# Kernel optimization log

Measured on AMD Instinct MI355X. Metric: run time of the kernel, lower is better.

## Reference

```python
import jax, jax.numpy as jnp
import numpy as np

N, DIN, E, BLK = 16384, 128, 262144, 2048
H1, DH1, H2, DH2 = 4, 128, 4, 128
D, L, HT, OUT = 128, 5, 4, 2


def _gat(h_in, src, dst, W, a_s, a_d, b, concat):
    # PyG GATConv (eval mode, no dropout): message src->dst, softmax per dst
    H, Dh = a_s.shape
    h = (h_in @ W).reshape(N, H, Dh)
    als = jnp.einsum('nhd,hd->nh', h, a_s)
    ald = jnp.einsum('nhd,hd->nh', h, a_d)
    e = jax.nn.leaky_relu(als[src] + ald[dst], 0.2)            # [E2,H]
    m = jax.ops.segment_max(e, dst, num_segments=N)
    ex = jnp.exp(e - m[dst])
    den = jax.ops.segment_sum(ex, dst, num_segments=N)
    alpha = ex / (den[dst] + 1e-16)
    out = jax.ops.segment_sum(alpha[:, :, None] * h[src], dst, num_segments=N)
    return (out.reshape(N, H * Dh) if concat else out.mean(axis=1)) + b


def _pe():
    pos = jnp.arange(L, dtype=jnp.float32)[:, None]
    div = jnp.exp(jnp.arange(0, D, 2, dtype=jnp.float32) * (-jnp.log(10000.0) / D))
    return jnp.zeros((L, D)).at[:, 0::2].set(jnp.sin(pos * div)).at[:, 1::2].set(jnp.cos(pos * div))


def reference(x, edge_index, time_step, W1, a_src1, a_dst1, b1, W2, a_src2, a_dst2, b2,
              wq, bq, wk, bk, wv, bv, wo, bo, ln_g, ln_b, f1, fb1, f2, fb2, wc, bc):
    s, d = edge_index[0], edge_index[1]
    loops = jnp.arange(N, dtype=edge_index.dtype)
    src = jnp.concatenate([s, d, loops])
    dst = jnp.concatenate([d, s, loops])

    # structural encoder (two GAT layers)
    h = jax.nn.elu(_gat(x, src, dst, W1, a_src1, a_dst1, b1, True))
    h2 = _gat(h, src, dst, W2, a_src2, a_dst2, b2, False)       # [N, D]

    # temporal self-attention: banks are empty (one snapshot per node), so
    # seq has only the last slot valid; original detaches seq before temporal.
    seq = jnp.zeros((N, L, D), h2.dtype).at[:, L - 1].set(jax.lax.stop_gradient(h2))
    xs = seq + _pe()[None]                                       # [N,L,D]
    dh = D // HT
    q = xs[:, -1]                                                # only last query is used
    Q = (q @ wq + bq).reshape(N, HT, dh)
    K = (xs @ wk + bk).reshape(N, L, HT, dh)
    V = (xs @ wv + bv).reshape(N, L, HT, dh)
    scores = jnp.einsum('nhd,nlhd->nhl', Q, K) / jnp.sqrt(jnp.float32(dh))
    valid = (jnp.arange(L) == L - 1)                             # key_padding_mask: pad except last
    scores = jnp.where(valid[None, None, :], scores, -1e9)
    attn = jax.nn.softmax(scores, axis=-1)
    ctx = jnp.einsum('nhl,nlhd->nhd', attn, V).reshape(N, D)
    ao = ctx @ wo + bo

    def ln(v):
        mu = v.mean(-1, keepdims=True)
        var = v.var(-1, keepdims=True)
        return (v - mu) / jnp.sqrt(var + 1e-5) * ln_g + ln_b

    y = ln(q + ao)
    y = ln(y + jax.nn.relu(y @ f1 + fb1) @ f2 + fb2)
    return y @ wc + bc                                           # [N, 2]


def setup_inputs():
    key = jax.random.key(0)
    ks = jax.random.split(key, 20)
    src = jax.random.randint(ks[0], (E,), 0, N, dtype=jnp.int32)
    off = jax.random.randint(ks[1], (E,), 0, BLK, dtype=jnp.int32)
    dst = (src // BLK) * BLK + off                               # within-snapshot edges
    r = lambda k, shape, s=0.05: jax.random.normal(k, shape, jnp.float32) * s
    return {
        'x': jax.random.normal(ks[2], (N, DIN), jnp.float32),
        'edge_index': jnp.stack([src, dst]),
        'time_step': (jnp.arange(N) // BLK).astype(jnp.int64),
        'W1': r(ks[3], (DIN, H1 * DH1)), 'a_src1': r(ks[4], (H1, DH1)), 'a_dst1': r(ks[5], (H1, DH1)), 'b1': jnp.zeros((H1 * DH1,)),
        'W2': r(ks[6], (H1 * DH1, H2 * DH2)), 'a_src2': r(ks[7], (H2, DH2)), 'a_dst2': r(ks[8], (H2, DH2)), 'b2': jnp.zeros((DH2,)),
        'wq': r(ks[9], (D, D)), 'bq': jnp.zeros((D,)), 'wk': r(ks[10], (D, D)), 'bk': jnp.zeros((D,)),
        'wv': r(ks[11], (D, D)), 'bv': jnp.zeros((D,)), 'wo': r(ks[12], (D, D)), 'bo': jnp.zeros((D,)),
        'ln_g': jnp.ones((D,)), 'ln_b': jnp.zeros((D,)),
        'f1': r(ks[13], (D, 4 * D)), 'fb1': jnp.zeros((4 * D,)), 'f2': r(ks[14], (4 * D, D)), 'fb2': jnp.zeros((D,)),
        'wc': r(ks[15], (D, OUT)), 'bc': jnp.zeros((OUT,)),
    }
```

## Files before the change

### kernel.cpp

```cpp
#include <hip/hip_runtime.h>
#include <hip/hip_bf16.h>

#define NODES 16384
#define FEAT 512
typedef __hip_bfloat16 bf16;
typedef __hip_bfloat162 bf162;
typedef short short8v __attribute__((ext_vector_type(8)));
typedef float f32x4 __attribute__((ext_vector_type(4)));

static __device__ __forceinline__ float b2f(short s){
  return __uint_as_float(((unsigned)(unsigned short)s) << 16);
}
static __device__ __forceinline__ void split_store(bf16* h, bf16* l, size_t i, float v){
  bf16 hi = __float2bfloat16(v);
  h[i] = hi; l[i] = __float2bfloat16(v - __bfloat162float(hi));
}

__global__ void sentinel_kernel(float* __restrict__ out, int n, float v){
  int i = blockIdx.x*blockDim.x + threadIdx.x;
  if (i < n) out[i] = v;
}

__global__ void zero_kernel(int* __restrict__ p, int n){
  int i = blockIdx.x*blockDim.x + threadIdx.x;
  if (i < n) p[i] = 0;
}
__global__ void count_kernel(const int* __restrict__ ei, int* __restrict__ counts, int E){
  int i = blockIdx.x*blockDim.x + threadIdx.x;
  if (i < 2*E){
    int dst = (i < E) ? ei[E+i] : ei[i-E];
    atomicAdd(&counts[dst], 1);
  }
}
__global__ __launch_bounds__(1024) void scan_kernel(const int* __restrict__ counts,
                                                    int* __restrict__ offs, int* __restrict__ cursor){
  __shared__ int sh[1024];
  const int t = threadIdx.x;
  int loc[16]; int s = 0;
#pragma unroll
  for (int i=0;i<16;i++){ loc[i] = counts[t*16+i]; s += loc[i]; }
  sh[t] = s; __syncthreads();
  for (int d=1; d<1024; d<<=1){
    int v = (t>=d) ? sh[t-d] : 0;
    __syncthreads(); sh[t] += v; __syncthreads();
  }
  int run = (t==0) ? 0 : sh[t-1];
#pragma unroll
  for (int i=0;i<16;i++){ offs[t*16+i] = run; cursor[t*16+i] = run; run += loc[i]; }
  if (t==1023) offs[NODES] = run;
}
__global__ void fill_kernel(const int* __restrict__ ei, int* __restrict__ cursor,
                            unsigned short* __restrict__ csr, int E){
  int i = blockIdx.x*blockDim.x + threadIdx.x;
  if (i < 2*E){
    int src = ei[i];
    int dst = (i < E) ? ei[E+i] : ei[i-E];
    int pos = atomicAdd(&cursor[dst], 1);
    csr[pos] = (unsigned short)src;
  }
}

struct PrepArgs {
  const float *x,*W1,*W2,*wv,*wo,*f1,*f2;
  bf16 *xh,*w1h,*w2h,*wvh,*wvl,*woh,*wol,*f1h,*f1l,*f2h,*f2l;
};
__global__ void prep_kernel(PrepArgs P){
  int i = blockIdx.x*blockDim.x + threadIdx.x;
  if (i < 2097152){ P.xh[i] = __float2bfloat16(P.x[i]); return; }
  i -= 2097152;
  if (i < 65536){ P.w1h[i] = __float2bfloat16(P.W1[(i&127)*512 + (i>>7)]); return; }
  i -= 65536;
  if (i < 262144){ P.w2h[i] = __float2bfloat16(P.W2[(i&511)*512 + (i>>9)]); return; }
  i -= 262144;
  if (i < 16384){ split_store(P.wvh, P.wvl, i, P.wv[(i&127)*128 + (i>>7)]); return; }
  i -= 16384;
  if (i < 16384){ split_store(P.woh, P.wol, i, P.wo[(i&127)*128 + (i>>7)]); return; }
  i -= 16384;
  if (i < 65536){ split_store(P.f1h, P.f1l, i, P.f1[(i&127)*512 + (i>>7)]); return; }
  i -= 65536;
  if (i < 65536){ split_store(P.f2h, P.f2l, i, P.f2[(i&511)*128 + (i>>9)]); return; }
}

static __device__ __forceinline__ short8v ld8(const bf16* p){
  return *(const short8v*)(const void*)(p);
}

template<int K>
__global__ __launch_bounds__(256) void lgemm(
    const bf16* __restrict__ A, const bf16* __restrict__ B,
    bf16* __restrict__ C, int N){
  __shared__ bf16 As[128*40];
  __shared__ bf16 Bs[128*40];
  const int tid = threadIdx.x;
  const int l = tid & 63, w = tid >> 6;
  const int lg = l >> 4, lr = l & 15;
  const int wr = w >> 1, wc = w & 1;
  const int r0 = blockIdx.x*128;
  const int c0 = blockIdx.y*128;
  const int srow = tid >> 1;
  const int spos = (tid & 1) * 16;
  f32x4 acc[4][4] = {};
  const int ardA[4] = { (wr*64 +  0 + lr)*40 + lg*8, (wr*64 + 16 + lr)*40 + lg*8,
                        (wr*64 + 32 + lr)*40 + lg*8, (wr*64 + 48 + lr)*40 + lg*8 };
  const int brdB[4] = { (wc*64 +  0 + lr)*40 + lg*8, (wc*64 + 16 + lr)*40 + lg*8,
                        (wc*64 + 32 + lr)*40 + lg*8, (wc*64 + 48 + lr)*40 + lg*8 };
  const size_t agbase = (size_t)(r0 + srow)*K + spos;
  const size_t bgbase = (size_t)(c0 + srow)*K + spos;
  const int sl = srow*40 + spos;
#pragma unroll
  for (int k0 = 0; k0 < K; k0 += 32){
    *(short8v*)&As[sl]     = ld8(A + agbase + k0);
    *(short8v*)&As[sl + 8] = ld8(A + agbase + k0 + 8);
    *(short8v*)&Bs[sl]     = ld8(B + bgbase + k0);
    *(short8v*)&Bs[sl + 8] = ld8(B + bgbase + k0 + 8);
    __syncthreads();
    short8v af[4], bfr[4];
#pragma unroll
    for (int f=0; f<4; f++){
      af[f]  = *(const short8v*)&As[ardA[f]];
      bfr[f] = *(const short8v*)&Bs[brdB[f]];
    }
#pragma unroll
    for (int fm=0; fm<4; fm++)
#pragma unroll
      for (int fn=0; fn<4; fn++)
        acc[fm][fn] = __builtin_amdgcn_mfma_f32_16x16x32_bf16(af[fm], bfr[fn], acc[fm][fn], 0,0,0);
    __syncthreads();
  }
#pragma unroll
  for (int fm=0; fm<4; fm++){
#pragma unroll
    for (int fn=0; fn<4; fn++){
      const int col = c0 + wc*64 + fn*16 + lr;
#pragma unroll
      for (int r=0; r<4; r++){
        const int row = r0 + wr*64 + fm*16 + lg*4 + r;
        C[(size_t)row*N + col] = __float2bfloat16(acc[fm][fn][r]);
      }
    }
  }
}

template<int K, int SA, int SB, int ACT, int OMODE, int WPB>
__global__ __launch_bounds__(256) void mgemm(
    const bf16* __restrict__ Ah, const bf16* __restrict__ Al,
    const bf16* __restrict__ Bh, const bf16* __restrict__ Bl,
    const float* __restrict__ bias,
    float* __restrict__ Cf, bf16* __restrict__ Ch, bf16* __restrict__ Cl, int N){
  const int l = threadIdx.x & 63, w = threadIdx.x >> 6;
  const int lg = l >> 4, lr = l & 15;
  const int r0 = (blockIdx.x*WPB + w)*64;
  const int c0 = blockIdx.y*64;
  f32x4 acc[4][4] = {};
  int abase[4], bbase[4];
#pragma unroll
  for (int f=0; f<4; f++){
    abase[f] = (r0 + f*16 + lr)*K + lg*8;
    bbase[f] = (c0 + f*16 + lr)*K + lg*8;
  }
#pragma unroll
  for (int k0 = 0; k0 < K; k0 += 32){
    short8v ah[4], alo[4], bh[4], blo[4];
#pragma unroll
    for (int f=0; f<4; f++){
      ah[f] = ld8(Ah + abase[f] + k0);
      if (SA) alo[f] = ld8(Al + abase[f] + k0);
      bh[f] = ld8(Bh + bbase[f] + k0);
      if (SB) blo[f] = ld8(Bl + bbase[f] + k0);
    }
#pragma unroll
    for (int fm=0; fm<4; fm++)
#pragma unroll
      for (int fn=0; fn<4; fn++){
        acc[fm][fn] = __builtin_amdgcn_mfma_f32_16x16x32_bf16(ah[fm], bh[fn], acc[fm][fn], 0,0,0);
        if (SB) acc[fm][fn] = __builtin_amdgcn_mfma_f32_16x16x32_bf16(ah[fm], blo[fn], acc[fm][fn], 0,0,0);
        if (SA) acc[fm][fn] = __builtin_amdgcn_mfma_f32_16x16x32_bf16(alo[fm], bh[fn], acc[fm][fn], 0,0,0);
      }
  }
#pragma unroll
  for (int fm=0; fm<4; fm++){
#pragma unroll
    for (int fn=0; fn<4; fn++){
      const int col = c0 + fn*16 + lr;
      const float bv = bias ? bias[col] : 0.f;
#pragma unroll
      for (int r=0; r<4; r++){
        const int row = r0 + fm*16 + lg*4 + r;
        float v = acc[fm][fn][r] + bv;
        if (ACT==1) v = fmaxf(v, 0.f);
        const size_t idx = (size_t)row*N + col;
        if (OMODE==0) Cf[idx] = v;
        else if (OMODE==1) Ch[idx] = __float2bfloat16(v);
        else split_store(Ch, Cl, idx, v);
      }
    }
  }
}

__global__ __launch_bounds__(256) void alsald_kernel(const bf16* __restrict__ h,
    const float* __restrict__ a_s, const float* __restrict__ a_d,
    float* __restrict__ als, float* __restrict__ ald){
  int n = blockIdx.x;
  int w = threadIdx.x >> 6, lane = threadIdx.x & 63;
  int c = w*128 + lane*2;
  bf162 hv = *(const bf162*)&h[(size_t)n*FEAT + c];
  float hx = __bfloat162float(hv.x), hy = __bfloat162float(hv.y);
  float2 as2 = *(const float2*)&a_s[c];
  float2 ad2 = *(const float2*)&a_d[c];
  float s = hx*as2.x + hy*as2.y;
  float d = hx*ad2.x + hy*ad2.y;
#pragma unroll
  for (int o=32;o>0;o>>=1){ s += __shfl_xor(s,o); d += __shfl_xor(d,o); }
  if (lane == 0){ als[n*4+w] = s; ald[n*4+w] = d; }
}

template<bool CONCAT>
__global__ __launch_bounds__(256) void gat_fused_kernel(const bf16* __restrict__ hfeat,
    const float* __restrict__ als, const float* __restrict__ ald,
    const int* __restrict__ offs, const unsigned short* __restrict__ csr,
    const float* __restrict__ bias, void* __restrict__ outv,
    bf16* __restrict__ qh, bf16* __restrict__ ql){
  const int w = threadIdx.x >> 6, l = threadIdx.x & 63, g = l >> 4, s16 = l & 15;
  const int nb = blockIdx.x;
  const int n = (nb & 7)*2048 + (nb >> 3)*4 + w;
  const float adg = ald[(size_t)n*4 + g];
  const int beg = offs[n];
  const int cnt = offs[n+1] - beg + 1;
  float ev[6]; int sv[6];
#pragma unroll
  for (int p=0;p<6;p++){
    const int i = s16 + p*16;
    int src = n;
    float e = -1e30f;
    if (i < cnt){
      if (i < cnt-1) src = (int)csr[beg+i];
      float t = als[(size_t)src*4+g] + adg;
      e = fmaxf(t, 0.2f*t);
    }
    ev[p] = e; sv[p] = src;
  }
  float m = -1e30f;
#pragma unroll
  for (int p=0;p<6;p++) m = fmaxf(m, ev[p]);
  float den = 0.f;
#pragma unroll
  for (int p=0;p<6;p++) den += (ev[p] > -1e29f) ? __expf(ev[p]-m) : 0.f;
#pragma unroll
  for (int mask=1; mask<16; mask<<=1){
    float mo = __shfl_xor(m, mask);
    float dd = __shfl_xor(den, mask);
    float nm = fmaxf(m, mo);
    den = den*__expf(m-nm) + dd*__expf(mo-nm);
    m = nm;
  }
  const float C = __expf(-m)/(den + 1e-16f);
  int pk[6];
#pragma unroll
  for (int p=0;p<6;p++){
    float a = (ev[p] > -1e29f) ? __expf(ev[p])*C : 0.f;
    bf16 ab = __float2bfloat16(a);
    pk[p] = ((int)*(unsigned short*)&ab << 16) | (sv[p] & 0xFFFF);
  }
  float acc[8] = {0,0,0,0,0,0,0,0};
  const int fb = l*8;
  const bf16* hp = hfeat + fb;
#pragma unroll
  for (int p=0;p<6;p++){
    const int pbase = p*16;
    if (pbase < cnt){
      const int lim = (cnt - pbase < 16) ? (cnt - pbase) : 16;
      int u_c = __shfl(pk[p], (l & 48));
      short8v hv_c = *(const short8v*)(const void*)(hp + (size_t)(u_c & 0xFFFF)*FEAT);
      for (int j=1; j<lim; ++j){
        const int u_n = __shfl(pk[p], (l & 48) | j);
        const short8v hv_n = *(const short8v*)(const void*)(hp + (size_t)(u_n & 0xFFFF)*FEAT);
        const float a_c = __uint_as_float((unsigned)u_c & 0xFFFF0000u);
#pragma unroll
        for (int k=0;k<8;k++) acc[k] += a_c * b2f(hv_c[k]);
        u_c = u_n; hv_c = hv_n;
      }
      const float a_c = __uint_as_float((unsigned)u_c & 0xFFFF0000u);
#pragma unroll
      for (int k=0;k<8;k++) acc[k] += a_c * b2f(hv_c[k]);
    }
  }
  for (int i = 96; i < cnt; ++i){
    const int src = (i < cnt-1) ? (int)csr[beg+i] : n;
    float t = als[(size_t)src*4+g] + adg;
    t = fmaxf(t, 0.2f*t);
    const float a = __expf(t)*C;
    const short8v hv = *(const short8v*)(const void*)&hfeat[(size_t)src*FEAT + fb];
#pragma unroll
    for (int k=0;k<8;k++) acc[k] += a * b2f(hv[k]);
  }
  if (CONCAT){
    short8v ov;
#pragma unroll
    for (int j=0;j<8;j++){
      float v = acc[j] + bias[fb+j];
      v = v > 0.f ? v : expm1f(v);
      bf16 bv = __float2bfloat16(v);
      ov[j] = (short)*(unsigned short*)&bv;
    }
    *(short8v*)((char*)outv + ((size_t)n*FEAT + fb)*2) = ov;
  } else {
#pragma unroll
    for (int j=0;j<8;j++){
      acc[j] += __shfl_xor(acc[j], 16);
      acc[j] += __shfl_xor(acc[j], 32);
    }
    if (l < 16){
      float* op = (float*)outv + (size_t)n*128 + l*8;
#pragma unroll
      for (int j=0;j<8;j++){
        const int col = l*8 + j;
        float v = 0.25f*acc[j] + bias[col];
        float ex = __expf((float)(col & ~1) * (-9.210340371976184f/128.f));
        float pe = (col & 1) ? cosf(4.f*ex) : sinf(4.f*ex);
        float q = v + pe;
        op[j] = q;
        split_store(qh, ql, (size_t)n*128 + col, q);
      }
    }
  }
}

template<int SPLIT>
__global__ __launch_bounds__(256) void ln_kernel(const float* __restrict__ a, const float* __restrict__ b,
    const float* __restrict__ g, const float* __restrict__ bb, float* __restrict__ out,
    bf16* __restrict__ oh, bf16* __restrict__ ol){
  int row = blockIdx.x*4 + (threadIdx.x >> 6);
  int lane = threadIdx.x & 63;
  int c = lane*2;
  float2 va = *(const float2*)&a[(size_t)row*128 + c];
  float2 vb = *(const float2*)&b[(size_t)row*128 + c];
  float x0 = va.x+vb.x, x1 = va.y+vb.y;
  float s = x0+x1, q = x0*x0 + x1*x1;
#pragma unroll
  for (int o=32;o>0;o>>=1){ s += __shfl_xor(s,o); q += __shfl_xor(q,o); }
  float mu = s*(1.f/128.f);
  float var = q*(1.f/128.f) - mu*mu;
  float r = 1.f/sqrtf(var + 1e-5f);
  float y0 = (x0-mu)*r*g[c]   + bb[c];
  float y1 = (x1-mu)*r*g[c+1] + bb[c+1];
  size_t idx = (size_t)row*128 + c;
  out[idx] = y0; out[idx+1] = y1;
  if (SPLIT){ split_store(oh, ol, idx, y0); split_store(oh, ol, idx+1, y1); }
}

__global__ __launch_bounds__(256) void ln_final_kernel(const float* __restrict__ a, const float* __restrict__ b,
    const float* __restrict__ g, const float* __restrict__ bb,
    const float* __restrict__ wc, const float* __restrict__ bc,
    float* __restrict__ out){
  int row = blockIdx.x*4 + (threadIdx.x >> 6);
  int lane = threadIdx.x & 63;
  int c = lane*2;
  float2 va = *(const float2*)&a[(size_t)row*128 + c];
  float2 vb = *(const float2*)&b[(size_t)row*128 + c];
  float x0 = va.x+vb.x, x1 = va.y+vb.y;
  float s = x0+x1, q = x0*x0 + x1*x1;
#pragma unroll
  for (int o=32;o>0;o>>=1){ s += __shfl_xor(s,o); q += __shfl_xor(q,o); }
  float mu = s*(1.f/128.f);
  float var = q*(1.f/128.f) - mu*mu;
  float r = 1.f/sqrtf(var + 1e-5f);
  float y0 = (x0-mu)*r*g[c]   + bb[c];
  float y1 = (x1-mu)*r*g[c+1] + bb[c+1];
  float s0 = y0*wc[c*2]   + y1*wc[(c+1)*2];
  float s1 = y0*wc[c*2+1] + y1*wc[(c+1)*2+1];
#pragma unroll
  for (int o=32;o>0;o>>=1){ s0 += __shfl_xor(s0,o); s1 += __shfl_xor(s1,o); }
  if (lane == 0){
    out[row*2]   = s0 + bc[0];
    out[row*2+1] = s1 + bc[1];
  }
}

extern "C" void kernel_launch(void* const* d_in, const int* in_sizes, int n_in,
                              void* d_out, int out_size, void* d_ws, size_t ws_size,
                              hipStream_t stream){
  const float* x      = (const float*)d_in[0];
  const int*   ei     = (const int*)d_in[1];
  const float* W1     = (const float*)d_in[3];
  const float* a_src1 = (const float*)d_in[4];
  const float* a_dst1 = (const float*)d_in[5];
  const float* b1     = (const float*)d_in[6];
  const float* W2     = (const float*)d_in[7];
  const float* a_src2 = (const float*)d_in[8];
  const float* a_dst2 = (const float*)d_in[9];
  const float* b2     = (const float*)d_in[10];
  const float* wv     = (const float*)d_in[15];
  const float* bv     = (const float*)d_in[16];
  const float* wo     = (const float*)d_in[17];
  const float* bo     = (const float*)d_in[18];
  const float* ln_g   = (const float*)d_in[19];
  const float* ln_b   = (const float*)d_in[20];
  const float* f1     = (const float*)d_in[21];
  const float* fb1    = (const float*)d_in[22];
  const float* f2     = (const float*)d_in[23];
  const float* fb2    = (const float*)d_in[24];
  const float* wc     = (const float*)d_in[25];
  const float* bc     = (const float*)d_in[26];
  float* outp = (float*)d_out;

  const int E = in_sizes[1] / 2;
  const int n = NODES;
  const int tE = 2*E;
  const size_t MB = 1024*1024;

  const size_t NEED = 36*MB;
  if (ws_size < NEED){
    sentinel_kernel<<<(out_size+255)/256, 256, 0, stream>>>(outp, out_size,
        1000.0f + (float)(ws_size / MB));
    return;
  }

  char* base = (char*)d_ws;
  int* counts = (int*)(base + 0);
  int* cursor = (int*)(base + 65536);
  bf16*  h1    = (bf16*)(base + 0);
  bf16*  xh    = (bf16*)(base + 16*MB);
  bf16*  h     = (bf16*)(base + 16*MB);
  bf16*  h2f   = (bf16*)(base + 0);
  float* h2q   = (float*)(base + 16*MB);
  bf16*  qh    = (bf16*)(base + 24*MB);
  bf16*  ql    = (bf16*)(base + 28*MB);
  bf16*  vh    = (bf16*)(base + 0);
  bf16*  vl    = (bf16*)(base + 4*MB);
  float* aobuf = (float*)(base + 8*MB);
  float* y1    = (float*)(base + 24*MB);
  bf16*  y1h   = (bf16*)(base + 0);
  bf16*  y1l   = (bf16*)(base + 4*MB);
  bf16*  hidden= (bf16*)(base + 8*MB);
  float* ffn2f = (float*)(base + 0);
  char* u = base + 32*MB;
  bf16* w1h = (bf16*)u; u += 131072;
  bf16* w2h = (bf16*)u; u += 524288;
  bf16* wvh = (bf16*)u; u += 32768;   bf16* wvl = (bf16*)u; u += 32768;
  bf16* woh = (bf16*)u; u += 32768;   bf16* wol = (bf16*)u; u += 32768;
  bf16* f1h = (bf16*)u; u += 131072;  bf16* f1l = (bf16*)u; u += 131072;
  bf16* f2h = (bf16*)u; u += 131072;  bf16* f2l = (bf16*)u; u += 131072;
  float* als  = (float*)u; u += (size_t)n*4*4;
  float* ald  = (float*)u; u += (size_t)n*4*4;
  int* offs   = (int*)u;   u += (size_t)(n+1)*4 + 252;
  unsigned short* csr = (unsigned short*)u; u += (size_t)tE*2;

  PrepArgs P = { x,W1,W2,wv,wo,f1,f2, xh,w1h,w2h,wvh,wvl,woh,wol,f1h,f1l,f2h,f2l };
  prep_kernel<<<(2588672+255)/256, 256, 0, stream>>>(P);
  zero_kernel<<<(n+255)/256, 256, 0, stream>>>(counts, n);
  count_kernel<<<(tE+255)/256, 256, 0, stream>>>(ei, counts, E);
  scan_kernel<<<1, 1024, 0, stream>>>(counts, offs, cursor);
  fill_kernel<<<(tE+255)/256, 256, 0, stream>>>(ei, cursor, csr, E);

  lgemm<128><<<dim3(128,4), 256, 0, stream>>>(xh, w1h, h1, 512);
  alsald_kernel<<<n, 256, 0, stream>>>(h1, a_src1, a_dst1, als, ald);
  gat_fused_kernel<true><<<n/4, 256, 0, stream>>>(h1, als, ald, offs, csr, b1, h, nullptr, nullptr);

  lgemm<512><<<dim3(128,4), 256, 0, stream>>>(h, w2h, h2f, 512);
  alsald_kernel<<<n, 256, 0, stream>>>(h2f, a_src2, a_dst2, als, ald);
  gat_fused_kernel<false><<<n/4, 256, 0, stream>>>(h2f, als, ald, offs, csr, b2, h2q, qh, ql);

  mgemm<128,1,1,0,2,2><<<dim3(128,2), 128, 0, stream>>>(qh, ql, wvh, wvl, bv, nullptr, vh, vl, 128);
  mgemm<128,1,1,0,0,2><<<dim3(128,2), 128, 0, stream>>>(vh, vl, woh, wol, bo, aobuf, nullptr, nullptr, 128);
  ln_kernel<1><<<n/4, 256, 0, stream>>>(h2q, aobuf, ln_g, ln_b, y1, y1h, y1l);
  mgemm<128,1,1,1,1,4><<<dim3(64,8), 256, 0, stream>>>(y1h, y1l, f1h, f1l, fb1, nullptr, hidden, nullptr, 512);
  mgemm<512,0,1,0,0,2><<<dim3(128,2), 128, 0, stream>>>(hidden, nullptr, f2h, f2l, fb2, ffn2f, nullptr, nullptr, 128);
  ln_final_kernel<<<n/4, 256, 0, stream>>>(y1, ffn2f, ln_g, ln_b, wc, bc, outp);
}
```

Before: 299.2 us.

## Split GAT aggregation across two waves per node and tile weight transposes

The fused GAT kernel now uses two wavefronts per destination node instead of one. Each wave handles alternating 16-edge chunks, and the partial softmax statistics and accumulators are merged through shared memory with block barriers. This doubles the parallelism on the latency-bound gather, at the cost of extra syncs and shared-memory traffic. The prep kernel is also reorganized: x is converted in contiguous chunks and weight transposes go through a 64x64 shared tile, so both reads and writes are coalesced.

```diff
diff --git a/kernel.cpp b/kernel.cpp
--- a/kernel.cpp
+++ b/kernel.cpp
@@ -64,21 +64,42 @@
   const float *x,*W1,*W2,*wv,*wo,*f1,*f2;
   bf16 *xh,*w1h,*w2h,*wvh,*wvl,*woh,*wol,*f1h,*f1l,*f2h,*f2l;
 };
-__global__ void prep_kernel(PrepArgs P){
-  int i = blockIdx.x*blockDim.x + threadIdx.x;
-  if (i < 2097152){ P.xh[i] = __float2bfloat16(P.x[i]); return; }
-  i -= 2097152;
-  if (i < 65536){ P.w1h[i] = __float2bfloat16(P.W1[(i&127)*512 + (i>>7)]); return; }
-  i -= 65536;
-  if (i < 262144){ P.w2h[i] = __float2bfloat16(P.W2[(i&511)*512 + (i>>9)]); return; }
-  i -= 262144;
-  if (i < 16384){ split_store(P.wvh, P.wvl, i, P.wv[(i&127)*128 + (i>>7)]); return; }
-  i -= 16384;
-  if (i < 16384){ split_store(P.woh, P.wol, i, P.wo[(i&127)*128 + (i>>7)]); return; }
-  i -= 16384;
-  if (i < 65536){ split_store(P.f1h, P.f1l, i, P.f1[(i&127)*512 + (i>>7)]); return; }
-  i -= 65536;
-  if (i < 65536){ split_store(P.f2h, P.f2l, i, P.f2[(i&511)*128 + (i>>9)]); return; }
+__global__ __launch_bounds__(256) void prep_kernel(PrepArgs P){
+  const int b = blockIdx.x;
+  const int t = threadIdx.x;
+  if (b < 512){
+    const size_t base = (size_t)b*4096;
+#pragma unroll
+    for (int k=0;k<16;k++){
+      const size_t i = base + t + 256*k;
+      P.xh[i] = __float2bfloat16(P.x[i]);
+    }
+    return;
+  }
+  __shared__ float tile[64][65];
+  const float* src; bf16 *dh; bf16 *dl; int R, C, ti;
+  int bb = b - 512;
+  if (bb < 16){ src=P.W1; dh=P.w1h; dl=nullptr; R=128; C=512; ti=bb; }
+  else if ((bb-=16) < 64){ src=P.W2; dh=P.w2h; dl=nullptr; R=512; C=512; ti=bb; }
+  else if ((bb-=64) < 4){ src=P.wv; dh=P.wvh; dl=P.wvl; R=128; C=128; ti=bb; }
+  else if ((bb-=4) < 4){ src=P.wo; dh=P.woh; dl=P.wol; R=128; C=128; ti=bb; }
+  else if ((bb-=4) < 16){ src=P.f1; dh=P.f1h; dl=P.f1l; R=128; C=512; ti=bb; }
+  else { bb-=16; src=P.f2; dh=P.f2h; dl=P.f2l; R=512; C=128; ti=bb; }
+  const int ctiles = C/64;
+  const int r0 = (ti/ctiles)*64, c0 = (ti%ctiles)*64;
+  const int r = t >> 6, c = t & 63;
+#pragma unroll
+  for (int i=0;i<16;i++)
+    tile[r + 4*i][c] = src[(size_t)(r0 + r + 4*i)*C + c0 + c];
+  __syncthreads();
+#pragma unroll
+  for (int i=0;i<16;i++){
+    const int oc   = c0 + r + 4*i;
+    const int orow = r0 + c;
+    const float v = tile[c][r + 4*i];
+    const size_t oi = (size_t)oc*R + orow;
+    if (dl){ split_store(dh, dl, oi, v); } else { dh[oi] = __float2bfloat16(v); }
+  }
 }
 
 static __device__ __forceinline__ short8v ld8(const bf16* p){
@@ -220,31 +241,33 @@
     const int* __restrict__ offs, const unsigned short* __restrict__ csr,
     const float* __restrict__ bias, void* __restrict__ outv,
     bf16* __restrict__ qh, bf16* __restrict__ ql){
+  __shared__ float mdbuf[2][2][4][2];
+  __shared__ float mbuf[2][64][8];
   const int w = threadIdx.x >> 6, l = threadIdx.x & 63, g = l >> 4, s16 = l & 15;
+  const int half = w & 1, pair = w >> 1;
   const int nb = blockIdx.x;
-  const int n = (nb & 7)*2048 + (nb >> 3)*4 + w;
+  const int n = (nb & 7)*2048 + (nb >> 3)*2 + pair;
   const float adg = ald[(size_t)n*4 + g];
   const int beg = offs[n];
   const int cnt = offs[n+1] - beg + 1;
-  float ev[6]; int sv[6];
-#pragma unroll
-  for (int p=0;p<6;p++){
-    const int i = s16 + p*16;
+  float ev[3]; int sv[3];
+#pragma unroll
+  for (int i=0;i<3;i++){
+    const int p = half + 2*i;
+    const int idx = s16 + p*16;
     int src = n;
     float e = -1e30f;
-    if (i < cnt){
-      if (i < cnt-1) src = (int)csr[beg+i];
+    if (idx < cnt){
+      if (idx < cnt-1) src = (int)csr[beg+idx];
       float t = als[(size_t)src*4+g] + adg;
       e = fmaxf(t, 0.2f*t);
     }
-    ev[p] = e; sv[p] = src;
-  }
-  float m = -1e30f;
-#pragma unroll
-  for (int p=0;p<6;p++) m = fmaxf(m, ev[p]);
+    ev[i] = e; sv[i] = src;
+  }
+  float m = fmaxf(fmaxf(ev[0], ev[1]), ev[2]);
   float den = 0.f;
 #pragma unroll
-  for (int p=0;p<6;p++) den += (ev[p] > -1e29f) ? __expf(ev[p]-m) : 0.f;
+  for (int i=0;i<3;i++) den += (ev[i] > -1e29f) ? __expf(ev[i]-m) : 0.f;
 #pragma unroll
   for (int mask=1; mask<16; mask<<=1){
     float mo = __shfl_xor(m, mask);
@@ -253,26 +276,35 @@
     den = den*__expf(m-nm) + dd*__expf(mo-nm);
     m = nm;
   }
+  if (s16 == 0){ mdbuf[pair][half][g][0] = m; mdbuf[pair][half][g][1] = den; }
+  __syncthreads();
+  {
+    const float mo = mdbuf[pair][half^1][g][0];
+    const float dd = mdbuf[pair][half^1][g][1];
+    const float nm = fmaxf(m, mo);
+    den = den*__expf(m-nm) + dd*__expf(mo-nm);
+    m = nm;
+  }
   const float C = __expf(-m)/(den + 1e-16f);
-  int pk[6];
-#pragma unroll
-  for (int p=0;p<6;p++){
-    float a = (ev[p] > -1e29f) ? __expf(ev[p])*C : 0.f;
+  int pk[3];
+#pragma unroll
+  for (int i=0;i<3;i++){
+    float a = (ev[i] > -1e29f) ? __expf(ev[i])*C : 0.f;
     bf16 ab = __float2bfloat16(a);
-    pk[p] = ((int)*(unsigned short*)&ab << 16) | (sv[p] & 0xFFFF);
+    pk[i] = ((int)*(unsigned short*)&ab << 16) | (sv[i] & 0xFFFF);
   }
   float acc[8] = {0,0,0,0,0,0,0,0};
   const int fb = l*8;
   const bf16* hp = hfeat + fb;
 #pragma unroll
-  for (int p=0;p<6;p++){
-    const int pbase = p*16;
+  for (int i=0;i<3;i++){
+    const int pbase = (half + 2*i)*16;
     if (pbase < cnt){
       const int lim = (cnt - pbase < 16) ? (cnt - pbase) : 16;
-      int u_c = __shfl(pk[p], (l & 48));
+      int u_c = __shfl(pk[i], (l & 48));
       short8v hv_c = *(const short8v*)(const void*)(hp + (size_t)(u_c & 0xFFFF)*FEAT);
       for (int j=1; j<lim; ++j){
-        const int u_n = __shfl(pk[p], (l & 48) | j);
+        const int u_n = __shfl(pk[i], (l & 48) | j);
         const short8v hv_n = *(const short8v*)(const void*)(hp + (size_t)(u_n & 0xFFFF)*FEAT);
         const float a_c = __uint_as_float((unsigned)u_c & 0xFFFF0000u);
 #pragma unroll
@@ -284,15 +316,25 @@
       for (int k=0;k<8;k++) acc[k] += a_c * b2f(hv_c[k]);
     }
   }
-  for (int i = 96; i < cnt; ++i){
-    const int src = (i < cnt-1) ? (int)csr[beg+i] : n;
-    float t = als[(size_t)src*4+g] + adg;
-    t = fmaxf(t, 0.2f*t);
-    const float a = __expf(t)*C;
-    const short8v hv = *(const short8v*)(const void*)&hfeat[(size_t)src*FEAT + fb];
-#pragma unroll
-    for (int k=0;k<8;k++) acc[k] += a * b2f(hv[k]);
-  }
+  if (half == 0){
+    for (int i = 96; i < cnt; ++i){
+      const int src = (i < cnt-1) ? (int)csr[beg+i] : n;
+      float t = als[(size_t)src*4+g] + adg;
+      t = fmaxf(t, 0.2f*t);
+      const float a = __expf(t)*C;
+      const short8v hv = *(const short8v*)(const void*)&hfeat[(size_t)src*FEAT + fb];
+#pragma unroll
+      for (int k=0;k<8;k++) acc[k] += a * b2f(hv[k]);
+    }
+  }
+  if (half == 1){
+#pragma unroll
+    for (int k=0;k<8;k++) mbuf[pair][l][k] = acc[k];
+  }
+  __syncthreads();
+  if (half == 1) return;
+#pragma unroll
+  for (int k=0;k<8;k++) acc[k] += mbuf[pair][l][k];
   if (CONCAT){
     short8v ov;
 #pragma unroll
@@ -446,7 +488,7 @@
   unsigned short* csr = (unsigned short*)u; u += (size_t)tE*2;
 
   PrepArgs P = { x,W1,W2,wv,wo,f1,f2, xh,w1h,w2h,wvh,wvl,woh,wol,f1h,f1l,f2h,f2l };
-  prep_kernel<<<(2588672+255)/256, 256, 0, stream>>>(P);
+  prep_kernel<<<632, 256, 0, stream>>>(P);
   zero_kernel<<<(n+255)/256, 256, 0, stream>>>(counts, n);
   count_kernel<<<(tE+255)/256, 256, 0, stream>>>(ei, counts, E);
   scan_kernel<<<1, 1024, 0, stream>>>(counts, offs, cursor);
@@ -454,11 +496,11 @@
 
   lgemm<128><<<dim3(128,4), 256, 0, stream>>>(xh, w1h, h1, 512);
   alsald_kernel<<<n, 256, 0, stream>>>(h1, a_src1, a_dst1, als, ald);
-  gat_fused_kernel<true><<<n/4, 256, 0, stream>>>(h1, als, ald, offs, csr, b1, h, nullptr, nullptr);
+  gat_fused_kernel<true><<<n/2, 256, 0, stream>>>(h1, als, ald, offs, csr, b1, h, nullptr, nullptr);
 
   lgemm<512><<<dim3(128,4), 256, 0, stream>>>(h, w2h, h2f, 512);
   alsald_kernel<<<n, 256, 0, stream>>>(h2f, a_src2, a_dst2, als, ald);
-  gat_fused_kernel<false><<<n/4, 256, 0, stream>>>(h2f, als, ald, offs, csr, b2, h2q, qh, ql);
+  gat_fused_kernel<false><<<n/2, 256, 0, stream>>>(h2f, als, ald, offs, csr, b2, h2q, qh, ql);
 
   mgemm<128,1,1,0,2,2><<<dim3(128,2), 128, 0, stream>>>(qh, ql, wvh, wvl, bv, nullptr, vh, vl, 128);
   mgemm<128,1,1,0,0,2><<<dim3(128,2), 128, 0, stream>>>(vh, vl, woh, wol, bo, aobuf, nullptr, nullptr, 128);
```

After: 303.8 us. Within noise of the previous version (+1.5%).

## Route split-precision GEMMs through LDS-tiled kernel and tile weight transposes

Applied to the files above, without the earlier changes.

The register-direct mgemm, which loaded A and B fragments straight from global memory, is replaced by a generalized LDS-tiled lgemm with 128x128 tiles. It adds optional low-part operands for split-bf16 precision, bias, ReLU and the output modes. The prep kernel now transposes weights through a shared-memory tile for coalesced reads and writes, and converts x with per-block strided loops. The tiled GEMM cuts redundant global loads, but the 128-wide-N GEMMs launch only 128 blocks, which may underfill the GPU, and the extra LDS buffers raise shared-memory use.

```diff
diff --git a/kernel.cpp b/kernel.cpp
--- a/kernel.cpp
+++ b/kernel.cpp
@@ -64,33 +64,58 @@
   const float *x,*W1,*W2,*wv,*wo,*f1,*f2;
   bf16 *xh,*w1h,*w2h,*wvh,*wvl,*woh,*wol,*f1h,*f1l,*f2h,*f2l;
 };
-__global__ void prep_kernel(PrepArgs P){
-  int i = blockIdx.x*blockDim.x + threadIdx.x;
-  if (i < 2097152){ P.xh[i] = __float2bfloat16(P.x[i]); return; }
-  i -= 2097152;
-  if (i < 65536){ P.w1h[i] = __float2bfloat16(P.W1[(i&127)*512 + (i>>7)]); return; }
-  i -= 65536;
-  if (i < 262144){ P.w2h[i] = __float2bfloat16(P.W2[(i&511)*512 + (i>>9)]); return; }
-  i -= 262144;
-  if (i < 16384){ split_store(P.wvh, P.wvl, i, P.wv[(i&127)*128 + (i>>7)]); return; }
-  i -= 16384;
-  if (i < 16384){ split_store(P.woh, P.wol, i, P.wo[(i&127)*128 + (i>>7)]); return; }
-  i -= 16384;
-  if (i < 65536){ split_store(P.f1h, P.f1l, i, P.f1[(i&127)*512 + (i>>7)]); return; }
-  i -= 65536;
-  if (i < 65536){ split_store(P.f2h, P.f2l, i, P.f2[(i&511)*128 + (i>>9)]); return; }
+__global__ __launch_bounds__(256) void prep_kernel(PrepArgs P){
+  const int b = blockIdx.x;
+  const int t = threadIdx.x;
+  if (b < 512){
+    const size_t base = (size_t)b*4096;
+#pragma unroll
+    for (int k=0;k<16;k++){
+      const size_t i = base + t + 256*k;
+      P.xh[i] = __float2bfloat16(P.x[i]);
+    }
+    return;
+  }
+  __shared__ float tile[64][65];
+  const float* src; bf16 *dh; bf16 *dl; int R, C, ti;
+  int bb = b - 512;
+  if (bb < 16){ src=P.W1; dh=P.w1h; dl=nullptr; R=128; C=512; ti=bb; }
+  else if ((bb-=16) < 64){ src=P.W2; dh=P.w2h; dl=nullptr; R=512; C=512; ti=bb; }
+  else if ((bb-=64) < 4){ src=P.wv; dh=P.wvh; dl=P.wvl; R=128; C=128; ti=bb; }
+  else if ((bb-=4) < 4){ src=P.wo; dh=P.woh; dl=P.wol; R=128; C=128; ti=bb; }
+  else if ((bb-=4) < 16){ src=P.f1; dh=P.f1h; dl=P.f1l; R=128; C=512; ti=bb; }
+  else { bb-=16; src=P.f2; dh=P.f2h; dl=P.f2l; R=512; C=128; ti=bb; }
+  const int ctiles = C/64;
+  const int r0 = (ti/ctiles)*64, c0 = (ti%ctiles)*64;
+  const int r = t >> 6, c = t & 63;
+#pragma unroll
+  for (int i=0;i<16;i++)
+    tile[r + 4*i][c] = src[(size_t)(r0 + r + 4*i)*C + c0 + c];
+  __syncthreads();
+#pragma unroll
+  for (int i=0;i<16;i++){
+    const int oc   = c0 + r + 4*i;
+    const int orow = r0 + c;
+    const float v = tile[c][r + 4*i];
+    const size_t oi = (size_t)oc*R + orow;
+    if (dl){ split_store(dh, dl, oi, v); } else { dh[oi] = __float2bfloat16(v); }
+  }
 }
 
 static __device__ __forceinline__ short8v ld8(const bf16* p){
   return *(const short8v*)(const void*)(p);
 }
 
-template<int K>
+template<int K, int SA, int SB, int ACT, int OMODE>
 __global__ __launch_bounds__(256) void lgemm(
-    const bf16* __restrict__ A, const bf16* __restrict__ B,
-    bf16* __restrict__ C, int N){
+    const bf16* __restrict__ A, const bf16* __restrict__ Al,
+    const bf16* __restrict__ B, const bf16* __restrict__ Bl,
+    const float* __restrict__ bias,
+    float* __restrict__ Cf, bf16* __restrict__ Ch, bf16* __restrict__ Cl, int N){
   __shared__ bf16 As[128*40];
   __shared__ bf16 Bs[128*40];
+  __shared__ bf16 Asl[SA ? 128*40 : 1];
+  __shared__ bf16 Bsl[SB ? 128*40 : 1];
   const int tid = threadIdx.x;
   const int l = tid & 63, w = tid >> 6;
   const int lg = l >> 4, lr = l & 15;
@@ -100,10 +125,10 @@
   const int srow = tid >> 1;
   const int spos = (tid & 1) * 16;
   f32x4 acc[4][4] = {};
-  const int ardA[4] = { (wr*64 +  0 + lr)*40 + lg*8, (wr*64 + 16 + lr)*40 + lg*8,
-                        (wr*64 + 32 + lr)*40 + lg*8, (wr*64 + 48 + lr)*40 + lg*8 };
-  const int brdB[4] = { (wc*64 +  0 + lr)*40 + lg*8, (wc*64 + 16 + lr)*40 + lg*8,
-                        (wc*64 + 32 + lr)*40 + lg*8, (wc*64 + 48 + lr)*40 + lg*8 };
+  const int ard[4] = { (wr*64 +  0 + lr)*40 + lg*8, (wr*64 + 16 + lr)*40 + lg*8,
+                       (wr*64 + 32 + lr)*40 + lg*8, (wr*64 + 48 + lr)*40 + lg*8 };
+  const int brd[4] = { (wc*64 +  0 + lr)*40 + lg*8, (wc*64 + 16 + lr)*40 + lg*8,
+                       (wc*64 + 32 + lr)*40 + lg*8, (wc*64 + 48 + lr)*40 + lg*8 };
   const size_t agbase = (size_t)(r0 + srow)*K + spos;
   const size_t bgbase = (size_t)(c0 + srow)*K + spos;
   const int sl = srow*40 + spos;
@@ -113,18 +138,31 @@
     *(short8v*)&As[sl + 8] = ld8(A + agbase + k0 + 8);
     *(short8v*)&Bs[sl]     = ld8(B + bgbase + k0);
     *(short8v*)&Bs[sl + 8] = ld8(B + bgbase + k0 + 8);
+    if (SA){
+      *(short8v*)&Asl[sl]     = ld8(Al + agbase + k0);
+      *(short8v*)&Asl[sl + 8] = ld8(Al + agbase + k0 + 8);
+    }
+    if (SB){
+      *(short8v*)&Bsl[sl]     = ld8(Bl + bgbase + k0);
+      *(short8v*)&Bsl[sl + 8] = ld8(Bl + bgbase + k0 + 8);
+    }
     __syncthreads();
-    short8v af[4], bfr[4];
+    short8v af[4], bfr[4], afl[4], bfl[4];
 #pragma unroll
     for (int f=0; f<4; f++){
-      af[f]  = *(const short8v*)&As[ardA[f]];
-      bfr[f] = *(const short8v*)&Bs[brdB[f]];
+      af[f]  = *(const short8v*)&As[ard[f]];
+      bfr[f] = *(const short8v*)&Bs[brd[f]];
+      if (SA) afl[f] = *(const short8v*)&Asl[ard[f]];
+      if (SB) bfl[f] = *(const short8v*)&Bsl[brd[f]];
     }
 #pragma unroll
     for (int fm=0; fm<4; fm++)
 #pragma unroll
-      for (int fn=0; fn<4; fn++)
+      for (int fn=0; fn<4; fn++){
         acc[fm][fn] = __builtin_amdgcn_mfma_f32_16x16x32_bf16(af[fm], bfr[fn], acc[fm][fn], 0,0,0);
+        if (SB) acc[fm][fn] = __builtin_amdgcn_mfma_f32_16x16x32_bf16(af[fm], bfl[fn], acc[fm][fn], 0,0,0);
+        if (SA) acc[fm][fn] = __builtin_amdgcn_mfma_f32_16x16x32_bf16(afl[fm], bfr[fn], acc[fm][fn], 0,0,0);
+      }
     __syncthreads();
   }
 #pragma unroll
@@ -132,60 +170,10 @@
 #pragma unroll
     for (int fn=0; fn<4; fn++){
       const int col = c0 + wc*64 + fn*16 + lr;
+      const float bv = bias ? bias[col] : 0.f;
 #pragma unroll
       for (int r=0; r<4; r++){
         const int row = r0 + wr*64 + fm*16 + lg*4 + r;
-        C[(size_t)row*N + col] = __float2bfloat16(acc[fm][fn][r]);
-      }
-    }
-  }
-}
-
-template<int K, int SA, int SB, int ACT, int OMODE, int WPB>
-__global__ __launch_bounds__(256) void mgemm(
-    const bf16* __restrict__ Ah, const bf16* __restrict__ Al,
-    const bf16* __restrict__ Bh, const bf16* __restrict__ Bl,
-    const float* __restrict__ bias,
-    float* __restrict__ Cf, bf16* __restrict__ Ch, bf16* __restrict__ Cl, int N){
-  const int l = threadIdx.x & 63, w = threadIdx.x >> 6;
-  const int lg = l >> 4, lr = l & 15;
-  const int r0 = (blockIdx.x*WPB + w)*64;
-  const int c0 = blockIdx.y*64;
-  f32x4 acc[4][4] = {};
-  int abase[4], bbase[4];
-#pragma unroll
-  for (int f=0; f<4; f++){
-    abase[f] = (r0 + f*16 + lr)*K + lg*8;
-    bbase[f] = (c0 + f*16 + lr)*K + lg*8;
-  }
-#pragma unroll
-  for (int k0 = 0; k0 < K; k0 += 32){
-    short8v ah[4], alo[4], bh[4], blo[4];
-#pragma unroll
-    for (int f=0; f<4; f++){
-      ah[f] = ld8(Ah + abase[f] + k0);
-      if (SA) alo[f] = ld8(Al + abase[f] + k0);
-      bh[f] = ld8(Bh + bbase[f] + k0);
-      if (SB) blo[f] = ld8(Bl + bbase[f] + k0);
-    }
-#pragma unroll
-    for (int fm=0; fm<4; fm++)
-#pragma unroll
-      for (int fn=0; fn<4; fn++){
-        acc[fm][fn] = __builtin_amdgcn_mfma_f32_16x16x32_bf16(ah[fm], bh[fn], acc[fm][fn], 0,0,0);
-        if (SB) acc[fm][fn] = __builtin_amdgcn_mfma_f32_16x16x32_bf16(ah[fm], blo[fn], acc[fm][fn], 0,0,0);
-        if (SA) acc[fm][fn] = __builtin_amdgcn_mfma_f32_16x16x32_bf16(alo[fm], bh[fn], acc[fm][fn], 0,0,0);
-      }
-  }
-#pragma unroll
-  for (int fm=0; fm<4; fm++){
-#pragma unroll
-    for (int fn=0; fn<4; fn++){
-      const int col = c0 + fn*16 + lr;
-      const float bv = bias ? bias[col] : 0.f;
-#pragma unroll
-      for (int r=0; r<4; r++){
-        const int row = r0 + fm*16 + lg*4 + r;
         float v = acc[fm][fn][r] + bv;
         if (ACT==1) v = fmaxf(v, 0.f);
         const size_t idx = (size_t)row*N + col;
@@ -446,24 +434,24 @@
   unsigned short* csr = (unsigned short*)u; u += (size_t)tE*2;
 
   PrepArgs P = { x,W1,W2,wv,wo,f1,f2, xh,w1h,w2h,wvh,wvl,woh,wol,f1h,f1l,f2h,f2l };
-  prep_kernel<<<(2588672+255)/256, 256, 0, stream>>>(P);
+  prep_kernel<<<632, 256, 0, stream>>>(P);
   zero_kernel<<<(n+255)/256, 256, 0, stream>>>(counts, n);
   count_kernel<<<(tE+255)/256, 256, 0, stream>>>(ei, counts, E);
   scan_kernel<<<1, 1024, 0, stream>>>(counts, offs, cursor);
   fill_kernel<<<(tE+255)/256, 256, 0, stream>>>(ei, cursor, csr, E);
 
-  lgemm<128><<<dim3(128,4), 256, 0, stream>>>(xh, w1h, h1, 512);
+  lgemm<128,0,0,0,1><<<dim3(128,4), 256, 0, stream>>>(xh, nullptr, w1h, nullptr, nullptr, nullptr, h1, nullptr, 512);
   alsald_kernel<<<n, 256, 0, stream>>>(h1, a_src1, a_dst1, als, ald);
   gat_fused_kernel<true><<<n/4, 256, 0, stream>>>(h1, als, ald, offs, csr, b1, h, nullptr, nullptr);
 
-  lgemm<512><<<dim3(128,4), 256, 0, stream>>>(h, w2h, h2f, 512);
+  lgemm<512,0,0,0,1><<<dim3(128,4), 256, 0, stream>>>(h, nullptr, w2h, nullptr, nullptr, nullptr, h2f, nullptr, 512);
   alsald_kernel<<<n, 256, 0, stream>>>(h2f, a_src2, a_dst2, als, ald);
   gat_fused_kernel<false><<<n/4, 256, 0, stream>>>(h2f, als, ald, offs, csr, b2, h2q, qh, ql);
 
-  mgemm<128,1,1,0,2,2><<<dim3(128,2), 128, 0, stream>>>(qh, ql, wvh, wvl, bv, nullptr, vh, vl, 128);
-  mgemm<128,1,1,0,0,2><<<dim3(128,2), 128, 0, stream>>>(vh, vl, woh, wol, bo, aobuf, nullptr, nullptr, 128);
+  lgemm<128,1,1,0,2><<<dim3(128,1), 256, 0, stream>>>(qh, ql, wvh, wvl, bv, nullptr, vh, vl, 128);
+  lgemm<128,1,1,0,0><<<dim3(128,1), 256, 0, stream>>>(vh, vl, woh, wol, bo, aobuf, nullptr, nullptr, 128);
   ln_kernel<1><<<n/4, 256, 0, stream>>>(h2q, aobuf, ln_g, ln_b, y1, y1h, y1l);
-  mgemm<128,1,1,1,1,4><<<dim3(64,8), 256, 0, stream>>>(y1h, y1l, f1h, f1l, fb1, nullptr, hidden, nullptr, 512);
-  mgemm<512,0,1,0,0,2><<<dim3(128,2), 128, 0, stream>>>(hidden, nullptr, f2h, f2l, fb2, ffn2f, nullptr, nullptr, 128);
+  lgemm<128,1,1,1,1><<<dim3(128,4), 256, 0, stream>>>(y1h, y1l, f1h, f1l, fb1, nullptr, hidden, nullptr, 512);
+  lgemm<512,0,1,0,0><<<dim3(128,1), 256, 0, stream>>>(hidden, nullptr, f2h, f2l, fb2, ffn2f, nullptr, nullptr, 128);
   ln_final_kernel<<<n/4, 256, 0, stream>>>(y1, ffn2f, ln_g, ln_b, wc, bc, outp);
 }
```

Result: faster. 278.7 us (-6.9%).
